# Optimization experiments

Hardware: AMD Instinct MI355X
Metric: run time of the kernel (lower is better)

## Reference

```python
import jax, jax.numpy as jnp
import numpy as np

B, T = 64, 512
NTOKEN, NINP, NLAB, NHID, NCLASS = 50000, 256, 64, 512, 10


def _fq_signed(x, bits=8):
    # symmetric per-tensor int fake-quant with STE (Brevitas Int8*PerTensor style)
    qmax = float(2 ** (bits - 1) - 1)
    s = jnp.maximum(jnp.max(jnp.abs(x)), 1e-8) / qmax
    q = jnp.clip(jnp.round(x / s), -qmax - 1.0, qmax) * s
    return x + jax.lax.stop_gradient(q - x)


def _fq_unsigned(x, bits=8):
    # unsigned per-tensor fake-quant for sigmoid outputs (Uint8ActPerTensor)
    qmax = float(2 ** bits - 1)
    s = jnp.maximum(jnp.max(x), 1e-8) / qmax
    q = jnp.clip(jnp.round(x / s), 0.0, qmax) * s
    return x + jax.lax.stop_gradient(q - x)


def setup_inputs() -> dict:
    key = jax.random.key(0)
    ks = jax.random.split(key, 10)
    x = jax.random.randint(ks[0], (B, T), 0, NTOKEN)
    x_pred = jax.random.randint(ks[1], (B,), 0, NTOKEN)
    y_ext = jax.random.randint(ks[2], (B,), 0, NCLASS)
    initrange = 0.1
    emb_tok = jax.random.uniform(ks[3], (NTOKEN, NINP), minval=-initrange, maxval=initrange)
    emb_lab = jax.random.uniform(ks[4], (NCLASS, NLAB), minval=-initrange, maxval=initrange)
    din = NINP + NLAB
    k = 1.0 / np.sqrt(NHID)
    Wi = jax.random.uniform(ks[5], (4 * NHID, din), minval=-k, maxval=k)
    Wh = jax.random.uniform(ks[6], (4 * NHID, NHID), minval=-k, maxval=k)
    bi = jax.random.uniform(ks[7], (4 * NHID,), minval=-k, maxval=k)
    bh = jax.random.uniform(ks[8], (4 * NHID,), minval=-k, maxval=k)
    Wdec = jax.random.uniform(ks[9], (NTOKEN, NHID), minval=-initrange, maxval=initrange)
    return {"x": x, "x_pred": x_pred, "y_ext": y_ext, "emb_tok": emb_tok,
            "emb_lab": emb_lab, "Wi": Wi, "Wh": Wh, "bi": bi, "bh": bh, "Wdec": Wdec}


def _forward(x, x_pred, y_ext, emb_tok, emb_lab, Wi, Wh, bi, bh, Wdec):
    # quantized embeddings
    tok = _fq_signed(emb_tok)[x]                     # [B,T,NINP]
    lab = _fq_signed(emb_lab)[y_ext]                 # [B,NLAB]
    lab_t = jnp.broadcast_to(lab[:, None, :], (x.shape[0], x.shape[1], lab.shape[-1]))
    # concat_label='input': label embedding concatenated on feature dim, io-quantized
    inp = _fq_signed(jnp.concatenate([tok, lab_t], axis=-1))   # [B,T,NINP+NLAB]
    Wi_q, Wh_q = _fq_signed(Wi), _fq_signed(Wh)
    bias = bi + bh
    # precompute input contribution to all 4 gates
    xW = jnp.einsum('btd,gd->btg', inp, Wi_q) + bias  # [B,T,4H]
    H = Wh.shape[1]

    def step(carry, xw_t):
        h, c = carry
        gates = _fq_signed(xw_t + h @ Wh_q.T)        # gate-accumulator quant [B,4H]
        i_g, f_g, g_g, o_g = jnp.split(gates, 4, axis=-1)
        i = _fq_unsigned(jax.nn.sigmoid(i_g))
        f = _fq_unsigned(jax.nn.sigmoid(f_g))
        o = _fq_unsigned(jax.nn.sigmoid(o_g))
        g = _fq_signed(jnp.tanh(g_g))
        c = f * c + i * g
        h = _fq_signed(o * _fq_signed(jnp.tanh(c)))  # tanh quant then io quant
        return (h, c), h

    h0 = jnp.zeros((x.shape[0], H), inp.dtype)
    _, hs = jax.lax.scan(step, (h0, h0), jnp.swapaxes(xW, 0, 1))
    out_seq = jnp.swapaxes(hs, 0, 1)                 # [B,T,H]
    # (first + last hidden state) / 2
    result = (out_seq[:, 0, :] + out_seq[:, -1, :]) * 0.5
    logits = result @ _fq_signed(Wdec).T             # [B,NTOKEN]
    logp = jax.nn.log_softmax(logits, axis=-1)
    nll = -jnp.take_along_axis(logp, x_pred[:, None], axis=1)[:, 0]
    return jnp.mean(nll)                             # avg_loss=True


def reference(x, x_pred, y_ext, emb_tok, emb_lab, Wi, Wh, bi, bh, Wdec):
    return _forward(x, x_pred, y_ext, emb_tok, emb_lab, Wi, Wh, bi, bh, Wdec)
```

## Files before the change

### kernel.cpp

```cpp
#include <hip/hip_runtime.h>

typedef unsigned short u16;
typedef unsigned int u32;
typedef unsigned long long u64;
typedef short short8 __attribute__((ext_vector_type(8)));
typedef float f32x4 __attribute__((ext_vector_type(4)));

#define B_ 64
#define T_ 512
#define H_ 512
#define DIN_ 320
#define G4_ 2048
#define NTOK_ 50000
#define P_ 64

#define OFF_CTRL  0
#define OFF_FLAG1 1024
#define OFF_FLAG2 5120
#define OFF_FLAG3 9216
#define OFF_FLAG4 13312
#define OFF_NLL   17408
#define OFF_BIAS  17664
#define OFF_HBUF  26624
#define OFF_RESF  92160
#define OFF_WI8   223232
#define OFF_WH8   1533952
#define OFF_INP   3631104
#define OFF_LOG   24602624

__device__ inline u16 f2b_exact(float f) { return (u16)(__float_as_uint(f) >> 16); }
__device__ inline float fqv(float x, float s) { return fminf(fmaxf(rintf(x / s), -128.f), 127.f) * s; }
__device__ inline float sigm(float x) { return 1.f / (1.f + expf(-x)); }
__device__ inline float wredmax(float v) {
#pragma unroll
  for (int d = 1; d < 64; d <<= 1) v = fmaxf(v, __shfl_xor(v, d, 64));
  return v;
}
__device__ inline f32x4 MFMA(short8 a, short8 b, f32x4 c) {
  return __builtin_amdgcn_mfma_f32_16x16x32_bf16(a, b, c, 0, 0, 0);
}
__device__ inline float bredmax(float v, float* red) {
  int tid = threadIdx.x;
  red[tid] = v; __syncthreads();
  for (int s = 128; s > 0; s >>= 1) { if (tid < s) red[tid] = fmaxf(red[tid], red[tid + s]); __syncthreads(); }
  float r = red[0]; __syncthreads();
  return r;
}

__device__ inline void st_flag(u64* p, u64 v) {
  __hip_atomic_store(p, v, __ATOMIC_RELAXED, __HIP_MEMORY_SCOPE_AGENT);
}
__device__ inline u64 ld_flag(u64* p) {
  return __hip_atomic_load(p, __ATOMIC_RELAXED, __HIP_MEMORY_SCOPE_AGENT);
}
__device__ inline void st_h(u16* p, u16 v) {
  __hip_atomic_store(p, v, __ATOMIC_RELAXED, __HIP_MEMORY_SCOPE_AGENT);
}
__device__ inline u64 ld_h64(const u16* p) {
  return __hip_atomic_load((const u64*)p, __ATOMIC_RELAXED, __HIP_MEMORY_SCOPE_AGENT);
}

__global__ void kInit(u32* w32, u32* hbuf32) {
  int i = blockIdx.x * blockDim.x + threadIdx.x, st = gridDim.x * blockDim.x;
  for (int j = i; j < 4352; j += st) w32[j] = 0u;
  for (int j = i; j < B_ * H_ / 2; j += st) hbuf32[j] = 0u;
}

__global__ void kMaxAbs(const float* p, int n4, u32* slot) {
  __shared__ float red[256];
  int i0 = blockIdx.x * blockDim.x + threadIdx.x, st = gridDim.x * blockDim.x;
  float m = 0.f;
  const float4* p4 = (const float4*)p;
  for (int i = i0; i < n4; i += st) {
    float4 v = p4[i];
    m = fmaxf(fmaxf(m, fmaxf(fabsf(v.x), fabsf(v.y))), fmaxf(fabsf(v.z), fabsf(v.w)));
  }
  m = bredmax(m, red);
  if (threadIdx.x == 0) atomicMax(slot, __float_as_uint(m));
}

__global__ void kGatherMax(const int* x, const int* y, const float* emb_tok, const float* emb_lab, u32* ctrl) {
  __shared__ float red[256];
  int tid = threadIdx.x;
  float mt = 0.f, ml = 0.f;
  for (int p = blockIdx.x; p < B_ * T_; p += gridDim.x)
    mt = fmaxf(mt, fabsf(emb_tok[(size_t)x[p] * 256 + tid]));
  for (int p = blockIdx.x; p < B_; p += gridDim.x)
    if (tid < 64) ml = fmaxf(ml, fabsf(emb_lab[y[p] * 64 + tid]));
  float m = bredmax(mt, red);
  if (tid == 0) atomicMax(&ctrl[7], __float_as_uint(m));
  m = bredmax(ml, red);
  if (tid == 0) atomicMax(&ctrl[8], __float_as_uint(m));
}

__global__ void kScalars(u32* ctrl) {
  float* s = (float*)(ctrl + 16);
  float mt = __uint_as_float(ctrl[2]), ml = __uint_as_float(ctrl[3]);
  float mwi = __uint_as_float(ctrl[4]), mwh = __uint_as_float(ctrl[5]), mwd = __uint_as_float(ctrl[6]);
  float mtg = __uint_as_float(ctrl[7]), mlg = __uint_as_float(ctrl[8]);
  float s_tok = fmaxf(mt, 1e-8f) / 127.f, s_lab = fmaxf(ml, 1e-8f) / 127.f;
  s[0] = s_tok; s[1] = s_lab;
  s[2] = fmaxf(mwi, 1e-8f) / 127.f;
  s[3] = fmaxf(mwh, 1e-8f) / 127.f;
  s[4] = fmaxf(mwd, 1e-8f) / 127.f;
  float qt = fminf(rintf(mtg / s_tok), 127.f) * s_tok;
  float ql = fminf(rintf(mlg / s_lab), 127.f) * s_lab;
  s[5] = fmaxf(fmaxf(qt, ql), 1e-8f) / 127.f;
}

__global__ void kBuildInp(const int* x, const int* y, const float* emb_tok, const float* emb_lab,
                          const u32* ctrl, u16* inp) {
  const float* s = (const float*)(ctrl + 16);
  float s_tok = s[0], s_lab = s[1], s_inp = s[5];
  int p = blockIdx.x, b = p >> 9, t = p & 511, d = threadIdx.x;
  float v, s1;
  if (d < 256) { v = emb_tok[(size_t)x[p] * 256 + d]; s1 = s_tok; }
  else         { v = emb_lab[y[b] * 64 + (d - 256)];  s1 = s_lab; }
  float q1 = fminf(fmaxf(rintf(v / s1), -128.f), 127.f) * s1;
  float k2 = fminf(fmaxf(rintf(q1 / s_inp), -128.f), 127.f);
  inp[((size_t)t * B_ + b) * DIN_ + d] = f2b_exact(k2);
}

__global__ void kQuantW(const float* Wi, const float* Wh, const float* bi, const float* bh,
                        const u32* ctrl, u16* wi8, u16* wh8, float* biasF) {
  const float* s = (const float*)(ctrl + 16);
  float sWi = s[2], sWh = s[3];
  const int NA = G4_ * DIN_, NB = G4_ * H_;
  int i0 = blockIdx.x * blockDim.x + threadIdx.x, st = gridDim.x * blockDim.x;
  for (int i = i0; i < NA + NB + G4_; i += st) {
    if (i < NA) {
      wi8[i] = f2b_exact(fminf(fmaxf(rintf(Wi[i] / sWi), -128.f), 127.f));
    } else if (i < NA + NB) {
      int j = i - NA;
      wh8[j] = f2b_exact(fminf(fmaxf(rintf(Wh[j] / sWh), -128.f), 127.f));
    } else {
      int r = i - NA - NB;
      biasF[r] = bi[r] + bh[r];
    }
  }
}

__global__ __launch_bounds__(256, 1) void kScan(
    const u16* inp8, const u16* wi8, const u16* wh8, const float* biasF,
    const u32* ctrl, u64* flag1, u64* flag2, u64* flag3, u64* flag4,
    u16* hBuf, float* resF) {
  __shared__ u16 ldsWi[20 * 64 * 8];
  __shared__ u16 ldsWh[32 * 64 * 8];
  __shared__ float actT[32][66];
  __shared__ float biasT[32];
  __shared__ float sRed[4][8];

  const int tid = threadIdx.x, lane = tid & 63, wid = tid >> 6;
  const int quad = lane >> 4, l15 = lane & 15;
  const int blk = blockIdx.x, hb = blk * 8;
  const float* scal = (const float*)(ctrl + 16);
  const float sWi = scal[2], sWh = scal[3], s_inp = scal[5];
  const float sA = s_inp * sWi;

  for (int fid = wid; fid < 20; fid += 4) {
    int nt = fid / 10, ks = fid - nt * 10;
    int n = nt * 16 + l15, r = (n >> 3) * 512 + hb + (n & 7);
    *(uint4*)&ldsWi[(fid * 64 + lane) * 8] = *(const uint4*)(wi8 + (size_t)r * DIN_ + ks * 32 + quad * 8);
  }
  for (int fid = wid; fid < 32; fid += 4) {
    int nt = fid >> 4, ks = fid & 15;
    int n = nt * 16 + l15, r = (n >> 3) * 512 + hb + (n & 7);
    *(uint4*)&ldsWh[(fid * 64 + lane) * 8] = *(const uint4*)(wh8 + (size_t)r * H_ + ks * 32 + quad * 8);
  }
  if (tid < 32) { int r = (tid >> 3) * 512 + hb + (tid & 7); biasT[tid] = biasF[r]; }
  __syncthreads();

  const int m0 = wid * 16;
  const int jj0 = tid & 7, b0 = tid >> 3;
  const int jj1 = (tid + 256) & 7, b1 = (tid + 256) >> 3;
  float cReg[2] = {0.f, 0.f};
  float hFirst[2] = {0.f, 0.f};
  float s_h_prev = 1.0f;

  f32x4 nA0 = {0.f, 0.f, 0.f, 0.f}, nA1 = {0.f, 0.f, 0.f, 0.f};
  {
    const u16* ip = inp8 + ((size_t)(m0 + l15)) * DIN_ + quad * 8;
#pragma unroll
    for (int ks = 0; ks < 10; ++ks) {
      short8 a = *(const short8*)(ip + ks * 32);
      nA0 = MFMA(a, *(const short8*)&ldsWi[(ks * 64 + lane) * 8], nA0);
      nA1 = MFMA(a, *(const short8*)&ldsWi[((10 + ks) * 64 + lane) * 8], nA1);
    }
  }

  for (int t = 0; t < T_; ++t) {
    const u32 sq = (u32)(t * 4);
    f32x4 aA0 = nA0, aA1 = nA1;

    if (t > 0) {
      u64* f4 = flag4 + lane * 8;
      for (;;) {
        u64 v = ld_flag(f4);
        if ((u32)(v >> 32) == sq) break;
        __builtin_amdgcn_s_sleep(4);
      }
      __builtin_amdgcn_sched_barrier(0);
    }

    f32x4 aB0 = {0.f,0.f,0.f,0.f}, aB1 = {0.f,0.f,0.f,0.f};
    const u16* hp = hBuf + (size_t)(m0 + l15) * H_ + quad * 8;
#pragma unroll
    for (int ks = 0; ks < 16; ++ks) {
      u64 w0 = ld_h64(hp + ks * 32);
      u64 w1 = ld_h64(hp + ks * 32 + 4);
      short8 a;
      ((u64*)&a)[0] = w0;
      ((u64*)&a)[1] = w1;
      aB0 = MFMA(a, *(const short8*)&ldsWh[(ks * 64 + lane) * 8], aB0);
      aB1 = MFMA(a, *(const short8*)&ldsWh[((16 + ks) * 64 + lane) * 8], aB1);
    }
    const float sB_ = s_h_prev * sWh;
    float vabs = 0.f, v0mx = -3e38f, v1mx = -3e38f, v1mn = 3e38f;
#pragma unroll
    for (int reg = 0; reg < 4; ++reg) {
      int m = m0 + quad * 4 + reg;
      float p0 = biasT[l15] + sA * aA0[reg] + sB_ * aB0[reg];
      float p1 = biasT[16 + l15] + sA * aA1[reg] + sB_ * aB1[reg];
      actT[l15][m] = p0; actT[16 + l15][m] = p1;
      vabs = fmaxf(vabs, fmaxf(fabsf(p0), fabsf(p1)));
      v0mx = fmaxf(v0mx, p0);
      v1mx = fmaxf(v1mx, p1);
      v1mn = fminf(v1mn, p1);
    }
    bool lo = (l15 < 8);
    float q[6];
    q[0] = vabs;
    q[1] = lo ? v0mx : -3e38f;
    q[2] = lo ? -3e38f : v0mx;
    q[3] = lo ? -3e38f : v1mx;
    q[4] = lo ? v1mx : -3e38f;
    q[5] = lo ? -v1mn : -3e38f;
#pragma unroll
    for (int d = 1; d < 64; d <<= 1) {
#pragma unroll
      for (int k = 0; k < 6; ++k) q[k] = fmaxf(q[k], __shfl_xor(q[k], d, 64));
    }
    if (lane == 0) {
#pragma unroll
      for (int k = 0; k < 6; ++k) sRed[wid][k] = q[k];
    }
    __syncthreads();
    if (tid < 6) {
      float m = fmaxf(fmaxf(sRed[0][tid], sRed[1][tid]), fmaxf(sRed[2][tid], sRed[3][tid]));
      st_flag(flag1 + blk * 8 + tid, (((u64)(sq + 1)) << 32) | (u64)__float_as_uint(m));
    }
    u64 a0, a1, a2, a3, a4, a5;
    {
      u64* fb = flag1 + lane * 8;
      const u32 e = sq + 1;
      for (;;) {
        a0 = ld_flag(fb + 0); a1 = ld_flag(fb + 1); a2 = ld_flag(fb + 2);
        a3 = ld_flag(fb + 3); a4 = ld_flag(fb + 4); a5 = ld_flag(fb + 5);
        if ((u32)(a0 >> 32) == e && (u32)(a1 >> 32) == e && (u32)(a2 >> 32) == e &&
            (u32)(a3 >> 32) == e && (u32)(a4 >> 32) == e && (u32)(a5 >> 32) == e) break;
        __builtin_amdgcn_s_sleep(4);
      }
    }
    float g0 = __uint_as_float((u32)a0), g1 = __uint_as_float((u32)a1),
          g2 = __uint_as_float((u32)a2), g3 = __uint_as_float((u32)a3),
          g4 = __uint_as_float((u32)a4), g5 = __uint_as_float((u32)a5);
#pragma unroll
    for (int d = 1; d < 64; d <<= 1) {
      g0 = fmaxf(g0, __shfl_xor(g0, d, 64));
      g1 = fmaxf(g1, __shfl_xor(g1, d, 64));
      g2 = fmaxf(g2, __shfl_xor(g2, d, 64));
      g3 = fmaxf(g3, __shfl_xor(g3, d, 64));
      g4 = fmaxf(g4, __shfl_xor(g4, d, 64));
      g5 = fmaxf(g5, __shfl_xor(g5, d, 64));
    }
    const float s_g = fmaxf(g0, 1e-8f) / 127.f;
    const float mi = g1, mf = g2, mo = g3, mg = g4, mgn = -g5;
    const float s_i = fmaxf(sigm(fqv(mi, s_g)), 1e-8f) / 255.f;
    const float s_f = fmaxf(sigm(fqv(mf, s_g)), 1e-8f) / 255.f;
    const float s_o = fmaxf(sigm(fqv(mo, s_g)), 1e-8f) / 255.f;
    const float ga = fmaxf(fabsf(fqv(mg, s_g)), fabsf(fqv(mgn, s_g)));
    const float s_gt = fmaxf(tanhf(ga), 1e-8f) / 127.f;

    float oqv[2];
    {
      float vi = sigm(fqv(actT[jj0][b0], s_g));
      float vf = sigm(fqv(actT[8 + jj0][b0], s_g));
      float vg = tanhf(fqv(actT[16 + jj0][b0], s_g));
      float vo = sigm(fqv(actT[24 + jj0][b0], s_g));
      float iq = fminf(fmaxf(rintf(vi / s_i), 0.f), 255.f) * s_i;
      float fq = fminf(fmaxf(rintf(vf / s_f), 0.f), 255.f) * s_f;
      float gq = fminf(fmaxf(rintf(vg / s_gt), -128.f), 127.f) * s_gt;
      oqv[0] = fminf(fmaxf(rintf(vo / s_o), 0.f), 255.f) * s_o;
      cReg[0] = fq * cReg[0] + iq * gq;
      vi = sigm(fqv(actT[jj1][b1], s_g));
      vf = sigm(fqv(actT[8 + jj1][b1], s_g));
      vg = tanhf(fqv(actT[16 + jj1][b1], s_g));
      vo = sigm(fqv(actT[24 + jj1][b1], s_g));
      iq = fminf(fmaxf(rintf(vi / s_i), 0.f), 255.f) * s_i;
      fq = fminf(fmaxf(rintf(vf / s_f), 0.f), 255.f) * s_f;
      gq = fminf(fmaxf(rintf(vg / s_gt), -128.f), 127.f) * s_gt;
      oqv[1] = fminf(fmaxf(rintf(vo / s_o), 0.f), 255.f) * s_o;
      cReg[1] = fq * cReg[1] + iq * gq;
    }
    float lm = wredmax(fmaxf(fabsf(cReg[0]), fabsf(cReg[1])));
    if (lane == 0) sRed[wid][0] = lm;
    __syncthreads();
    if (tid == 0) {
      float m = fmaxf(fmaxf(sRed[0][0], sRed[1][0]), fmaxf(sRed[2][0], sRed[3][0]));
      st_flag(flag2 + blk * 8, (((u64)(sq + 2)) << 32) | (u64)__float_as_uint(m));
    }
    float maxc;
    {
      u64* f2 = flag2 + lane * 8;
      u64 v;
      for (;;) {
        v = ld_flag(f2);
        if ((u32)(v >> 32) == sq + 2) break;
        __builtin_amdgcn_s_sleep(4);
      }
      maxc = __uint_as_float((u32)v);
    }
#pragma unroll
    for (int d = 1; d < 64; d <<= 1) maxc = fmaxf(maxc, __shfl_xor(maxc, d, 64));
    const float s_t = fmaxf(tanhf(maxc), 1e-8f) / 127.f;

    float hpv[2];
    hpv[0] = oqv[0] * fqv(tanhf(cReg[0]), s_t);
    hpv[1] = oqv[1] * fqv(tanhf(cReg[1]), s_t);
    lm = wredmax(fmaxf(fabsf(hpv[0]), fabsf(hpv[1])));
    if (lane == 0) sRed[wid][0] = lm;
    __syncthreads();
    if (tid == 0) {
      float m = fmaxf(fmaxf(sRed[0][0], sRed[1][0]), fmaxf(sRed[2][0], sRed[3][0]));
      st_flag(flag3 + blk * 8, (((u64)(sq + 3)) << 32) | (u64)__float_as_uint(m));
    }
    float maxhp;
    {
      u64* f3 = flag3 + lane * 8;
      u64 v;
      for (;;) {
        v = ld_flag(f3);
        if ((u32)(v >> 32) == sq + 3) break;
        __builtin_amdgcn_s_sleep(4);
      }
      maxhp = __uint_as_float((u32)v);
    }
#pragma unroll
    for (int d = 1; d < 64; d <<= 1) maxhp = fmaxf(maxhp, __shfl_xor(maxhp, d, 64));
    const float s_h = fmaxf(maxhp, 1e-8f) / 127.f;

    {
      float hi = fminf(fmaxf(rintf(hpv[0] / s_h), -128.f), 127.f);
      st_h(hBuf + b0 * H_ + hb + jj0, f2b_exact(hi));
      float hv = hi * s_h;
      if (t == 0) hFirst[0] = hv;
      if (t == T_ - 1) resF[b0 * H_ + hb + jj0] = 0.5f * (hFirst[0] + hv);
      hi = fminf(fmaxf(rintf(hpv[1] / s_h), -128.f), 127.f);
      st_h(hBuf + b1 * H_ + hb + jj1, f2b_exact(hi));
      hv = hi * s_h;
      if (t == 0) hFirst[1] = hv;
      if (t == T_ - 1) resF[b1 * H_ + hb + jj1] = 0.5f * (hFirst[1] + hv);
    }
    s_h_prev = s_h;
    if (t < T_ - 1) {
      __syncthreads();
      if (tid == 0) st_flag(flag4 + blk * 8, (((u64)(sq + 4)) << 32) | 1u);
      nA0 = (f32x4){0.f, 0.f, 0.f, 0.f};
      nA1 = (f32x4){0.f, 0.f, 0.f, 0.f};
      const u16* ip = inp8 + ((size_t)(t + 1) * B_ + m0 + l15) * DIN_ + quad * 8;
#pragma unroll
      for (int ks = 0; ks < 10; ++ks) {
        short8 a = *(const short8*)(ip + ks * 32);
        nA0 = MFMA(a, *(const short8*)&ldsWi[(ks * 64 + lane) * 8], nA0);
        nA1 = MFMA(a, *(const short8*)&ldsWi[((10 + ks) * 64 + lane) * 8], nA1);
      }
    }
  }
}

__global__ __launch_bounds__(256) void kDecode(const float* resF, const float* Wdec,
                                               const u32* ctrl, float* logits) {
  const float sWd = ((const float*)(ctrl + 16))[4];
  int c = blockIdx.x * 256 + threadIdx.x;
  if (c >= NTOK_) return;
  const float4* wrow = (const float4*)(Wdec + (size_t)c * H_);
  float acc[64];
#pragma unroll
  for (int rr = 0; rr < 64; rr++) acc[rr] = 0.f;
  for (int k4 = 0; k4 < H_ / 4; k4++) {
    float4 w = wrow[k4];
    float w0 = fminf(fmaxf(rintf(w.x / sWd), -128.f), 127.f) * sWd;
    float w1 = fminf(fmaxf(rintf(w.y / sWd), -128.f), 127.f) * sWd;
    float w2 = fminf(fmaxf(rintf(w.z / sWd), -128.f), 127.f) * sWd;
    float w3 = fminf(fmaxf(rintf(w.w / sWd), -128.f), 127.f) * sWd;
    const float* rp = resF + k4 * 4;
#pragma unroll
    for (int rr = 0; rr < 64; rr++) {
      acc[rr] += rp[rr * H_ + 0] * w0 + rp[rr * H_ + 1] * w1 +
                 rp[rr * H_ + 2] * w2 + rp[rr * H_ + 3] * w3;
    }
  }
#pragma unroll
  for (int rr = 0; rr < 64; rr++) logits[(size_t)rr * NTOK_ + c] = acc[rr];
}

__global__ void kLoss(const float* logits, const int* x_pred, float* nll) {
  __shared__ float red[256];
  int b = blockIdx.x, tid = threadIdx.x;
  const float* row = logits + (size_t)b * NTOK_;
  float m = -3e38f;
  for (int i = tid; i < NTOK_; i += 256) m = fmaxf(m, row[i]);
  m = bredmax(m, red);
  float s = 0.f;
  for (int i = tid; i < NTOK_; i += 256) s += expf(row[i] - m);
  red[tid] = s; __syncthreads();
  for (int st = 128; st > 0; st >>= 1) { if (tid < st) red[tid] += red[tid + st]; __syncthreads(); }
  if (tid == 0) nll[b] = m + logf(red[0]) - row[x_pred[b]];
}

__global__ void kFinal(const float* nll, float* out) {
  float s = 0.f;
  for (int i = 0; i < B_; i++) s += nll[i];
  out[0] = s / 64.f;
}

extern "C" void kernel_launch(void* const* d_in, const int* in_sizes, int n_in,
                              void* d_out, int out_size, void* d_ws, size_t ws_size,
                              hipStream_t stream) {
  const int* x      = (const int*)d_in[0];
  const int* x_pred = (const int*)d_in[1];
  const int* y_ext  = (const int*)d_in[2];
  const float* emb_tok = (const float*)d_in[3];
  const float* emb_lab = (const float*)d_in[4];
  const float* Wi   = (const float*)d_in[5];
  const float* Wh   = (const float*)d_in[6];
  const float* bi   = (const float*)d_in[7];
  const float* bh   = (const float*)d_in[8];
  const float* Wdec = (const float*)d_in[9];

  char* W = (char*)d_ws;
  u32* ctrl    = (u32*)(W + OFF_CTRL);
  u64* flag1   = (u64*)(W + OFF_FLAG1);
  u64* flag2   = (u64*)(W + OFF_FLAG2);
  u64* flag3   = (u64*)(W + OFF_FLAG3);
  u64* flag4   = (u64*)(W + OFF_FLAG4);
  float* nll   = (float*)(W + OFF_NLL);
  float* biasF = (float*)(W + OFF_BIAS);
  u16* hBuf    = (u16*)(W + OFF_HBUF);
  float* resF  = (float*)(W + OFF_RESF);
  u16* wi8     = (u16*)(W + OFF_WI8);
  u16* wh8     = (u16*)(W + OFF_WH8);
  u16* inp     = (u16*)(W + OFF_INP);
  float* logits = (float*)(W + OFF_LOG);

  kInit<<<128, 256, 0, stream>>>(ctrl, (u32*)hBuf);
  kMaxAbs<<<1024, 256, 0, stream>>>(emb_tok, NTOK_ * 256 / 4, ctrl + 2);
  kMaxAbs<<<1, 256, 0, stream>>>(emb_lab, 10 * 64 / 4, ctrl + 3);
  kMaxAbs<<<320, 256, 0, stream>>>(Wi, G4_ * DIN_ / 4, ctrl + 4);
  kMaxAbs<<<512, 256, 0, stream>>>(Wh, G4_ * H_ / 4, ctrl + 5);
  kMaxAbs<<<1024, 256, 0, stream>>>(Wdec, NTOK_ * H_ / 4, ctrl + 6);
  kGatherMax<<<256, 256, 0, stream>>>(x, y_ext, emb_tok, emb_lab, ctrl);
  kScalars<<<1, 1, 0, stream>>>(ctrl);
  kBuildInp<<<B_ * T_, DIN_, 0, stream>>>(x, y_ext, emb_tok, emb_lab, ctrl, inp);
  kQuantW<<<4096, 256, 0, stream>>>(Wi, Wh, bi, bh, ctrl, wi8, wh8, biasF);

  kScan<<<P_, 256, 0, stream>>>(inp, wi8, wh8, biasF, ctrl, flag1, flag2, flag3, flag4, hBuf, resF);

  kDecode<<<(NTOK_ + 255) / 256, 256, 0, stream>>>(resF, Wdec, ctrl, logits);
  kLoss<<<B_, 256, 0, stream>>>(logits, x_pred, nll);
  kFinal<<<1, 1, 0, stream>>>(nll, (float*)d_out);
}
```

Baseline: 7.807 ms.

## Co-locate scan blocks on one XCC and sync through L2 with sc0 accesses

The scan kernel now launches 512 blocks, has each read its XCC id, and picks 64 blocks that all sit on the same XCC to run the recurrence. It probes with a timed flag handshake that those blocks are co-resident; if so, flag and hidden-state traffic uses sc0 loads and stores that only go as far as the shared L2, with shorter sleeps and batched inline-asm loads. Otherwise it falls back to the original agent-scope atomics on blocks 0..63. This is meant to cut per-step cross-XCC synchronisation latency across the 512 timesteps, at the cost of a startup election and probe phase and reliance on L2 coherence within one XCC.

```diff
diff --git a/kernel.cpp b/kernel.cpp
--- a/kernel.cpp
+++ b/kernel.cpp
@@ -13,20 +13,22 @@
 #define G4_ 2048
 #define NTOK_ 50000
 #define P_ 64
+#define LB_ 512
 
 #define OFF_CTRL  0
 #define OFF_FLAG1 1024
 #define OFF_FLAG2 5120
 #define OFF_FLAG3 9216
 #define OFF_FLAG4 13312
-#define OFF_NLL   17408
-#define OFF_BIAS  17664
-#define OFF_HBUF  26624
-#define OFF_RESF  92160
-#define OFF_WI8   223232
-#define OFF_WH8   1533952
-#define OFF_INP   3631104
-#define OFF_LOG   24602624
+#define OFF_PROBE 17408
+#define OFF_NLL   21504
+#define OFF_BIAS  21760
+#define OFF_HBUF  30720
+#define OFF_RESF  96256
+#define OFF_WI8   227328
+#define OFF_WH8   1538048
+#define OFF_INP   3635200
+#define OFF_LOG   24606720
 
 __device__ inline u16 f2b_exact(float f) { return (u16)(__float_as_uint(f) >> 16); }
 __device__ inline float fqv(float x, float s) { return fminf(fmaxf(rintf(x / s), -128.f), 127.f) * s; }
@@ -47,22 +49,72 @@
   return r;
 }
 
-__device__ inline void st_flag(u64* p, u64 v) {
+__device__ inline void stF_ag(u64* p, u64 v) {
   __hip_atomic_store(p, v, __ATOMIC_RELAXED, __HIP_MEMORY_SCOPE_AGENT);
 }
-__device__ inline u64 ld_flag(u64* p) {
+__device__ inline u64 ldF_ag(u64* p) {
   return __hip_atomic_load(p, __ATOMIC_RELAXED, __HIP_MEMORY_SCOPE_AGENT);
 }
-__device__ inline void st_h(u16* p, u16 v) {
+__device__ inline void st_h_ag(u16* p, u16 v) {
   __hip_atomic_store(p, v, __ATOMIC_RELAXED, __HIP_MEMORY_SCOPE_AGENT);
 }
-__device__ inline u64 ld_h64(const u16* p) {
+__device__ inline u64 ld_h64_ag(const u16* p) {
   return __hip_atomic_load((const u64*)p, __ATOMIC_RELAXED, __HIP_MEMORY_SCOPE_AGENT);
 }
+
+__device__ inline u64 ldF_l2(const u64* p) {
+  u64 v;
+  asm volatile("global_load_dwordx2 %0, %1, off sc0\n\ts_waitcnt vmcnt(0)"
+               : "=&v"(v) : "v"(p) : "memory");
+  return v;
+}
+__device__ inline void stF_l2(u64* p, u64 v) {
+  asm volatile("global_store_dwordx2 %0, %1, off sc0" :: "v"(p), "v"(v) : "memory");
+}
+__device__ inline void st_h_l2(u16* p, u32 v) {
+  asm volatile("global_store_short %0, %1, off sc0" :: "v"(p), "v"(v) : "memory");
+}
+
+#define LDH16_L2(HP)                                                       \
+  asm volatile(                                                            \
+    "global_load_dwordx4 %0, %16, off sc0\n\t"                             \
+    "global_load_dwordx4 %1, %16, off offset:64 sc0\n\t"                   \
+    "global_load_dwordx4 %2, %16, off offset:128 sc0\n\t"                  \
+    "global_load_dwordx4 %3, %16, off offset:192 sc0\n\t"                  \
+    "global_load_dwordx4 %4, %16, off offset:256 sc0\n\t"                  \
+    "global_load_dwordx4 %5, %16, off offset:320 sc0\n\t"                  \
+    "global_load_dwordx4 %6, %16, off offset:384 sc0\n\t"                  \
+    "global_load_dwordx4 %7, %16, off offset:448 sc0\n\t"                  \
+    "global_load_dwordx4 %8, %16, off offset:512 sc0\n\t"                  \
+    "global_load_dwordx4 %9, %16, off offset:576 sc0\n\t"                  \
+    "global_load_dwordx4 %10, %16, off offset:640 sc0\n\t"                 \
+    "global_load_dwordx4 %11, %16, off offset:704 sc0\n\t"                 \
+    "global_load_dwordx4 %12, %16, off offset:768 sc0\n\t"                 \
+    "global_load_dwordx4 %13, %16, off offset:832 sc0\n\t"                 \
+    "global_load_dwordx4 %14, %16, off offset:896 sc0\n\t"                 \
+    "global_load_dwordx4 %15, %16, off offset:960 sc0\n\t"                 \
+    "s_waitcnt vmcnt(0)"                                                   \
+    : "=&v"(hh0), "=&v"(hh1), "=&v"(hh2), "=&v"(hh3),                      \
+      "=&v"(hh4), "=&v"(hh5), "=&v"(hh6), "=&v"(hh7),                      \
+      "=&v"(hh8), "=&v"(hh9), "=&v"(hh10), "=&v"(hh11),                    \
+      "=&v"(hh12), "=&v"(hh13), "=&v"(hh14), "=&v"(hh15)                   \
+    : "v"(HP) : "memory")
+
+#define LDF6_L2(FB)                                                        \
+  asm volatile(                                                            \
+    "global_load_dwordx2 %0, %6, off sc0\n\t"                              \
+    "global_load_dwordx2 %1, %6, off offset:8 sc0\n\t"                     \
+    "global_load_dwordx2 %2, %6, off offset:16 sc0\n\t"                    \
+    "global_load_dwordx2 %3, %6, off offset:24 sc0\n\t"                    \
+    "global_load_dwordx2 %4, %6, off offset:32 sc0\n\t"                    \
+    "global_load_dwordx2 %5, %6, off offset:40 sc0\n\t"                    \
+    "s_waitcnt vmcnt(0)"                                                   \
+    : "=&v"(a0), "=&v"(a1), "=&v"(a2), "=&v"(a3), "=&v"(a4), "=&v"(a5)     \
+    : "v"(FB) : "memory")
 
 __global__ void kInit(u32* w32, u32* hbuf32) {
   int i = blockIdx.x * blockDim.x + threadIdx.x, st = gridDim.x * blockDim.x;
-  for (int j = i; j < 4352; j += st) w32[j] = 0u;
+  for (int j = i; j < 5376; j += st) w32[j] = 0u;
   for (int j = i; j < B_ * H_ / 2; j += st) hbuf32[j] = 0u;
 }
 
@@ -140,36 +192,15 @@
   }
 }
 
-__global__ __launch_bounds__(256, 1) void kScan(
-    const u16* inp8, const u16* wi8, const u16* wh8, const float* biasF,
-    const u32* ctrl, u64* flag1, u64* flag2, u64* flag3, u64* flag4,
-    u16* hBuf, float* resF) {
-  __shared__ u16 ldsWi[20 * 64 * 8];
-  __shared__ u16 ldsWh[32 * 64 * 8];
-  __shared__ float actT[32][66];
-  __shared__ float biasT[32];
-  __shared__ float sRed[4][8];
-
+template <int L2M>
+__device__ void scanBody(const u16* inp8, u64* flag1, u64* flag2, u64* flag3, u64* flag4,
+                         u16* hBuf, float* resF,
+                         const u16* ldsWi, const u16* ldsWh,
+                         float (*actT)[66], const float* biasT, float (*sRed)[8],
+                         int blk, float sA, float sWh) {
   const int tid = threadIdx.x, lane = tid & 63, wid = tid >> 6;
   const int quad = lane >> 4, l15 = lane & 15;
-  const int blk = blockIdx.x, hb = blk * 8;
-  const float* scal = (const float*)(ctrl + 16);
-  const float sWi = scal[2], sWh = scal[3], s_inp = scal[5];
-  const float sA = s_inp * sWi;
-
-  for (int fid = wid; fid < 20; fid += 4) {
-    int nt = fid / 10, ks = fid - nt * 10;
-    int n = nt * 16 + l15, r = (n >> 3) * 512 + hb + (n & 7);
-    *(uint4*)&ldsWi[(fid * 64 + lane) * 8] = *(const uint4*)(wi8 + (size_t)r * DIN_ + ks * 32 + quad * 8);
-  }
-  for (int fid = wid; fid < 32; fid += 4) {
-    int nt = fid >> 4, ks = fid & 15;
-    int n = nt * 16 + l15, r = (n >> 3) * 512 + hb + (n & 7);
-    *(uint4*)&ldsWh[(fid * 64 + lane) * 8] = *(const uint4*)(wh8 + (size_t)r * H_ + ks * 32 + quad * 8);
-  }
-  if (tid < 32) { int r = (tid >> 3) * 512 + hb + (tid & 7); biasT[tid] = biasF[r]; }
-  __syncthreads();
-
+  const int hb = blk * 8;
   const int m0 = wid * 16;
   const int jj0 = tid & 7, b0 = tid >> 3;
   const int jj1 = (tid + 256) & 7, b1 = (tid + 256) >> 3;
@@ -195,24 +226,38 @@
     if (t > 0) {
       u64* f4 = flag4 + lane * 8;
       for (;;) {
-        u64 v = ld_flag(f4);
+        u64 v = L2M ? ldF_l2(f4) : ldF_ag(f4);
         if ((u32)(v >> 32) == sq) break;
-        __builtin_amdgcn_s_sleep(4);
+        __builtin_amdgcn_s_sleep(L2M ? 1 : 4);
       }
       __builtin_amdgcn_sched_barrier(0);
     }
 
     f32x4 aB0 = {0.f,0.f,0.f,0.f}, aB1 = {0.f,0.f,0.f,0.f};
     const u16* hp = hBuf + (size_t)(m0 + l15) * H_ + quad * 8;
-#pragma unroll
-    for (int ks = 0; ks < 16; ++ks) {
-      u64 w0 = ld_h64(hp + ks * 32);
-      u64 w1 = ld_h64(hp + ks * 32 + 4);
-      short8 a;
-      ((u64*)&a)[0] = w0;
-      ((u64*)&a)[1] = w1;
-      aB0 = MFMA(a, *(const short8*)&ldsWh[(ks * 64 + lane) * 8], aB0);
-      aB1 = MFMA(a, *(const short8*)&ldsWh[((16 + ks) * 64 + lane) * 8], aB1);
+    if constexpr (L2M) {
+      short8 hh0, hh1, hh2, hh3, hh4, hh5, hh6, hh7;
+      short8 hh8, hh9, hh10, hh11, hh12, hh13, hh14, hh15;
+      LDH16_L2(hp);
+#define MMK(K, HK)                                                         \
+      aB0 = MFMA(HK, *(const short8*)&ldsWh[((K) * 64 + lane) * 8], aB0);  \
+      aB1 = MFMA(HK, *(const short8*)&ldsWh[(((K) + 16) * 64 + lane) * 8], aB1);
+      MMK(0, hh0)  MMK(1, hh1)  MMK(2, hh2)  MMK(3, hh3)
+      MMK(4, hh4)  MMK(5, hh5)  MMK(6, hh6)  MMK(7, hh7)
+      MMK(8, hh8)  MMK(9, hh9)  MMK(10, hh10) MMK(11, hh11)
+      MMK(12, hh12) MMK(13, hh13) MMK(14, hh14) MMK(15, hh15)
+#undef MMK
+    } else {
+#pragma unroll
+      for (int ks = 0; ks < 16; ++ks) {
+        u64 w0 = ld_h64_ag(hp + ks * 32);
+        u64 w1 = ld_h64_ag(hp + ks * 32 + 4);
+        short8 a;
+        ((u64*)&a)[0] = w0;
+        ((u64*)&a)[1] = w1;
+        aB0 = MFMA(a, *(const short8*)&ldsWh[(ks * 64 + lane) * 8], aB0);
+        aB1 = MFMA(a, *(const short8*)&ldsWh[((16 + ks) * 64 + lane) * 8], aB1);
+      }
     }
     const float sB_ = s_h_prev * sWh;
     float vabs = 0.f, v0mx = -3e38f, v1mx = -3e38f, v1mn = 3e38f;
@@ -247,18 +292,23 @@
     __syncthreads();
     if (tid < 6) {
       float m = fmaxf(fmaxf(sRed[0][tid], sRed[1][tid]), fmaxf(sRed[2][tid], sRed[3][tid]));
-      st_flag(flag1 + blk * 8 + tid, (((u64)(sq + 1)) << 32) | (u64)__float_as_uint(m));
+      u64 pv = (((u64)(sq + 1)) << 32) | (u64)__float_as_uint(m);
+      if (L2M) stF_l2(flag1 + blk * 8 + tid, pv); else stF_ag(flag1 + blk * 8 + tid, pv);
     }
     u64 a0, a1, a2, a3, a4, a5;
     {
       u64* fb = flag1 + lane * 8;
       const u32 e = sq + 1;
       for (;;) {
-        a0 = ld_flag(fb + 0); a1 = ld_flag(fb + 1); a2 = ld_flag(fb + 2);
-        a3 = ld_flag(fb + 3); a4 = ld_flag(fb + 4); a5 = ld_flag(fb + 5);
+        if constexpr (L2M) {
+          LDF6_L2(fb);
+        } else {
+          a0 = ldF_ag(fb + 0); a1 = ldF_ag(fb + 1); a2 = ldF_ag(fb + 2);
+          a3 = ldF_ag(fb + 3); a4 = ldF_ag(fb + 4); a5 = ldF_ag(fb + 5);
+        }
         if ((u32)(a0 >> 32) == e && (u32)(a1 >> 32) == e && (u32)(a2 >> 32) == e &&
             (u32)(a3 >> 32) == e && (u32)(a4 >> 32) == e && (u32)(a5 >> 32) == e) break;
-        __builtin_amdgcn_s_sleep(4);
+        __builtin_amdgcn_s_sleep(L2M ? 1 : 4);
       }
     }
     float g0 = __uint_as_float((u32)a0), g1 = __uint_as_float((u32)a1),
@@ -307,16 +357,17 @@
     __syncthreads();
     if (tid == 0) {
       float m = fmaxf(fmaxf(sRed[0][0], sRed[1][0]), fmaxf(sRed[2][0], sRed[3][0]));
-      st_flag(flag2 + blk * 8, (((u64)(sq + 2)) << 32) | (u64)__float_as_uint(m));
+      u64 pv = (((u64)(sq + 2)) << 32) | (u64)__float_as_uint(m);
+      if (L2M) stF_l2(flag2 + blk * 8, pv); else stF_ag(flag2 + blk * 8, pv);
     }
     float maxc;
     {
       u64* f2 = flag2 + lane * 8;
       u64 v;
       for (;;) {
-        v = ld_flag(f2);
+        v = L2M ? ldF_l2(f2) : ldF_ag(f2);
         if ((u32)(v >> 32) == sq + 2) break;
-        __builtin_amdgcn_s_sleep(4);
+        __builtin_amdgcn_s_sleep(L2M ? 1 : 4);
       }
       maxc = __uint_as_float((u32)v);
     }
@@ -332,16 +383,17 @@
     __syncthreads();
     if (tid == 0) {
       float m = fmaxf(fmaxf(sRed[0][0], sRed[1][0]), fmaxf(sRed[2][0], sRed[3][0]));
-      st_flag(flag3 + blk * 8, (((u64)(sq + 3)) << 32) | (u64)__float_as_uint(m));
+      u64 pv = (((u64)(sq + 3)) << 32) | (u64)__float_as_uint(m);
+      if (L2M) stF_l2(flag3 + blk * 8, pv); else stF_ag(flag3 + blk * 8, pv);
     }
     float maxhp;
     {
       u64* f3 = flag3 + lane * 8;
       u64 v;
       for (;;) {
-        v = ld_flag(f3);
+        v = L2M ? ldF_l2(f3) : ldF_ag(f3);
         if ((u32)(v >> 32) == sq + 3) break;
-        __builtin_amdgcn_s_sleep(4);
+        __builtin_amdgcn_s_sleep(L2M ? 1 : 4);
       }
       maxhp = __uint_as_float((u32)v);
     }
@@ -351,20 +403,26 @@
 
     {
       float hi = fminf(fmaxf(rintf(hpv[0] / s_h), -128.f), 127.f);
-      st_h(hBuf + b0 * H_ + hb + jj0, f2b_exact(hi));
+      if (L2M) st_h_l2(hBuf + b0 * H_ + hb + jj0, (u32)f2b_exact(hi));
+      else     st_h_ag(hBuf + b0 * H_ + hb + jj0, f2b_exact(hi));
       float hv = hi * s_h;
       if (t == 0) hFirst[0] = hv;
       if (t == T_ - 1) resF[b0 * H_ + hb + jj0] = 0.5f * (hFirst[0] + hv);
       hi = fminf(fmaxf(rintf(hpv[1] / s_h), -128.f), 127.f);
-      st_h(hBuf + b1 * H_ + hb + jj1, f2b_exact(hi));
+      if (L2M) st_h_l2(hBuf + b1 * H_ + hb + jj1, (u32)f2b_exact(hi));
+      else     st_h_ag(hBuf + b1 * H_ + hb + jj1, f2b_exact(hi));
       hv = hi * s_h;
       if (t == 0) hFirst[1] = hv;
       if (t == T_ - 1) resF[b1 * H_ + hb + jj1] = 0.5f * (hFirst[1] + hv);
     }
     s_h_prev = s_h;
     if (t < T_ - 1) {
+      if (L2M) asm volatile("s_waitcnt vmcnt(0)" ::: "memory");
       __syncthreads();
-      if (tid == 0) st_flag(flag4 + blk * 8, (((u64)(sq + 4)) << 32) | 1u);
+      if (tid == 0) {
+        u64 pv = (((u64)(sq + 4)) << 32) | 1u;
+        if (L2M) stF_l2(flag4 + blk * 8, pv); else stF_ag(flag4 + blk * 8, pv);
+      }
       nA0 = (f32x4){0.f, 0.f, 0.f, 0.f};
       nA1 = (f32x4){0.f, 0.f, 0.f, 0.f};
       const u16* ip = inp8 + ((size_t)(t + 1) * B_ + m0 + l15) * DIN_ + quad * 8;
@@ -376,6 +434,116 @@
       }
     }
   }
+}
+
+__global__ __launch_bounds__(256, 2) void kScan(
+    const u16* inp8, const u16* wi8, const u16* wh8, const float* biasF,
+    u32* ctrl, u64* flag1, u64* flag2, u64* flag3, u64* flag4, u64* probeF,
+    u16* hBuf, float* resF) {
+  __shared__ u16 ldsWi[20 * 64 * 8];
+  __shared__ u16 ldsWh[32 * 64 * 8];
+  __shared__ float actT[32][66];
+  __shared__ float biasT[32];
+  __shared__ float sRed[4][8];
+  __shared__ int sInfo[2];
+
+  const int tid = threadIdx.x;
+
+  if (tid == 0) {
+    u32 xcc;
+    asm volatile("s_getreg_b32 %0, hwreg(HW_REG_XCC_ID)" : "=s"(xcc));
+    xcc &= 7u;
+    u32 rank = __hip_atomic_fetch_add(&ctrl[24 + xcc], 1u, __ATOMIC_RELAXED, __HIP_MEMORY_SCOPE_AGENT);
+    __hip_atomic_fetch_add(&ctrl[36], 1u, __ATOMIC_RELEASE, __HIP_MEMORY_SCOPE_AGENT);
+    if (blockIdx.x == 0) {
+      while (__hip_atomic_load(&ctrl[36], __ATOMIC_ACQUIRE, __HIP_MEMORY_SCOPE_AGENT) < (u32)LB_)
+        __builtin_amdgcn_s_sleep(8);
+      u32 pick = 0;
+      for (u32 x2 = 0; x2 < 8; ++x2) {
+        u32 c = __hip_atomic_load(&ctrl[24 + x2], __ATOMIC_RELAXED, __HIP_MEMORY_SCOPE_AGENT);
+        if (c >= (u32)P_) { pick = x2 + 1u; break; }
+      }
+      __hip_atomic_store(&ctrl[33], pick, __ATOMIC_RELAXED, __HIP_MEMORY_SCOPE_AGENT);
+    }
+    u32 pick;
+    for (;;) {
+      pick = __hip_atomic_load(&ctrl[33], __ATOMIC_RELAXED, __HIP_MEMORY_SCOPE_AGENT);
+      if (pick) break;
+      __builtin_amdgcn_s_sleep(8);
+    }
+    sInfo[0] = (pick != 0 && xcc == pick - 1u && rank < (u32)P_) ? (int)rank : -1;
+  }
+  __syncthreads();
+  const int cand = sInfo[0];
+
+  if (cand >= 0) {
+    const int lane = tid & 63, wid = tid >> 6;
+    if (tid == 0) stF_l2(probeF + cand * 8, (1ULL << 48) | 1ULL);
+    u64 t0 = __builtin_amdgcn_s_memrealtime();
+    int mine = 0;
+    for (;;) {
+      u64 v = ldF_l2(probeF + lane * 8);
+      if ((v >> 48) >= 1ULL) { mine = 1; break; }
+      if (__builtin_amdgcn_s_memrealtime() - t0 > 300000ULL) break;
+      __builtin_amdgcn_s_sleep(8);
+    }
+    if (tid == 0 && mine) stF_l2(probeF + cand * 8, (2ULL << 48) | 1ULL);
+    int mine2 = 0;
+    if (mine) {
+      t0 = __builtin_amdgcn_s_memrealtime();
+      for (;;) {
+        u64 v = ldF_l2(probeF + lane * 8);
+        if ((v >> 48) >= 2ULL) { mine2 = 1; break; }
+        if (__builtin_amdgcn_s_memrealtime() - t0 > 300000ULL) break;
+        __builtin_amdgcn_s_sleep(8);
+      }
+    }
+    int aw = __all(mine & mine2);
+    if (lane == 0) sRed[wid][0] = (float)aw;
+    __syncthreads();
+    if (tid == 0) {
+      int ok = (sRed[0][0] != 0.f) && (sRed[1][0] != 0.f) && (sRed[2][0] != 0.f) && (sRed[3][0] != 0.f);
+      if (!ok) __hip_atomic_fetch_or(&ctrl[34], 1u, __ATOMIC_RELAXED, __HIP_MEMORY_SCOPE_AGENT);
+      __hip_atomic_fetch_add(&ctrl[35], 1u, __ATOMIC_RELEASE, __HIP_MEMORY_SCOPE_AGENT);
+    }
+    __syncthreads();
+  }
+
+  if (tid == 0) {
+    while (__hip_atomic_load(&ctrl[35], __ATOMIC_ACQUIRE, __HIP_MEMORY_SCOPE_AGENT) < (u32)P_)
+      __builtin_amdgcn_s_sleep(8);
+    u32 fv = __hip_atomic_load(&ctrl[34], __ATOMIC_RELAXED, __HIP_MEMORY_SCOPE_AGENT);
+    sInfo[1] = (fv == 0u) ? 1 : 0;
+  }
+  __syncthreads();
+  const int l2mode = sInfo[1];
+  const int blk = l2mode ? cand : ((int)blockIdx.x < P_ ? (int)blockIdx.x : -1);
+  if (blk < 0) return;
+
+  const int lane = tid & 63, wid = tid >> 6;
+  const int quad = lane >> 4, l15 = lane & 15;
+  const int hb = blk * 8;
+  const float* scal = (const float*)(ctrl + 16);
+  const float sWi = scal[2], sWh = scal[3], s_inp = scal[5];
+  const float sA = s_inp * sWi;
+
+  for (int fid = wid; fid < 20; fid += 4) {
+    int nt = fid / 10, ks = fid - nt * 10;
+    int n = nt * 16 + l15, r = (n >> 3) * 512 + hb + (n & 7);
+    *(uint4*)&ldsWi[(fid * 64 + lane) * 8] = *(const uint4*)(wi8 + (size_t)r * DIN_ + ks * 32 + quad * 8);
+  }
+  for (int fid = wid; fid < 32; fid += 4) {
+    int nt = fid >> 4, ks = fid & 15;
+    int n = nt * 16 + l15, r = (n >> 3) * 512 + hb + (n & 7);
+    *(uint4*)&ldsWh[(fid * 64 + lane) * 8] = *(const uint4*)(wh8 + (size_t)r * H_ + ks * 32 + quad * 8);
+  }
+  if (tid < 32) { int r = (tid >> 3) * 512 + hb + (tid & 7); biasT[tid] = biasF[r]; }
+  __syncthreads();
+
+  if (l2mode)
+    scanBody<1>(inp8, flag1, flag2, flag3, flag4, hBuf, resF, ldsWi, ldsWh, actT, biasT, sRed, blk, sA, sWh);
+  else
+    scanBody<0>(inp8, flag1, flag2, flag3, flag4, hBuf, resF, ldsWi, ldsWh, actT, biasT, sRed, blk, sA, sWh);
 }
 
 __global__ __launch_bounds__(256) void kDecode(const float* resF, const float* Wdec,
@@ -444,6 +612,7 @@
   u64* flag2   = (u64*)(W + OFF_FLAG2);
   u64* flag3   = (u64*)(W + OFF_FLAG3);
   u64* flag4   = (u64*)(W + OFF_FLAG4);
+  u64* probeF  = (u64*)(W + OFF_PROBE);
   float* nll   = (float*)(W + OFF_NLL);
   float* biasF = (float*)(W + OFF_BIAS);
   u16* hBuf    = (u16*)(W + OFF_HBUF);
@@ -464,7 +633,8 @@
   kBuildInp<<<B_ * T_, DIN_, 0, stream>>>(x, y_ext, emb_tok, emb_lab, ctrl, inp);
   kQuantW<<<4096, 256, 0, stream>>>(Wi, Wh, bi, bh, ctrl, wi8, wh8, biasF);
 
-  kScan<<<P_, 256, 0, stream>>>(inp, wi8, wh8, biasF, ctrl, flag1, flag2, flag3, flag4, hBuf, resF);
+  kScan<<<LB_, 256, 0, stream>>>(inp, wi8, wh8, biasF, ctrl,
+                                 flag1, flag2, flag3, flag4, probeF, hBuf, resF);
 
   kDecode<<<(NTOK_ + 255) / 256, 256, 0, stream>>>(resF, Wdec, ctrl, logits);
   kLoss<<<B_, 256, 0, stream>>>(logits, x_pred, nll);
```

Measured after the change: 13.80 ms. 1.77x slower.
